# Performance work log

Measured on AMD Instinct MI355X. Metric: run time of the kernel, lower is better.

Reference implementation:

```python
import jax, jax.numpy as jnp
import numpy as np

V, D, M, C, L = 100000, 256, 4096, 4096, 32
PAD = 0
EPS = 1e-8  # torch CosineSimilarity default eps


def setup_inputs() -> dict:
    key = jax.random.key(0)
    ks = jax.random.split(key, 6)
    xs = jax.random.randint(ks[0], (1, L), 0, V)
    mems = jax.random.randint(ks[1], (M, L), 0, V)
    ys = jax.random.randint(ks[2], (1, L), 0, V)
    cands = jax.random.randint(ks[3], (C, L), 0, V)
    lt = jax.random.normal(ks[4], (V, D), dtype=jnp.float32) * 0.02
    lt = lt.at[PAD].set(0.0)  # nn.Embedding padding_idx row is zero
    freqs = jax.random.uniform(ks[5], (V,), dtype=jnp.float32, minval=0.05, maxval=1.0)
    return {"xs": xs, "mems": mems, "ys": ys, "cands": cands, "lt": lt, "freqs": freqs}


def _encode(tokens, lt, freqs):
    # Batched Encoder.forward: freq-weighted average of token embeddings.
    # tokens: [N, L] -> [N, D]
    emb = lt[tokens]                       # [N, L, D] gather
    w = freqs[tokens]                      # [N, L]
    w = w / jnp.linalg.norm(w, axis=1, keepdims=True)  # w * (1 / ||w||)
    return jnp.einsum('nl,nld->nd', w, emb)


def reference(xs, mems, ys, cands, lt, freqs):
    xs_emb = _encode(xs, lt, freqs)                                   # [1, D]
    mems_enc = jnp.concatenate([_encode(mems, lt, freqs), xs_emb], 0)  # [M+1, D]
    # cosine similarity of xs_emb (broadcast) against each memory row
    an = jnp.maximum(jnp.linalg.norm(xs_emb, axis=1), EPS)            # [1]
    bn = jnp.maximum(jnp.linalg.norm(mems_enc, axis=1), EPS)          # [M+1]
    cos = (mems_enc @ xs_emb[0]) / (an * bn)                          # [M+1]
    att = jax.nn.softmax(cos)[None, :]                                # [1, M+1]
    lhs_emb = att @ mems_enc                                          # [1, D]
    ys_emb = _encode(ys, lt, freqs)                                   # [1, D]
    cand_emb = _encode(cands, lt, freqs)                              # [C, D]
    # torch.cat of lhs_emb repeated (1 + C) times; ys then cand encodings
    xs_out = jnp.tile(lhs_emb, (cands.shape[0] + 1, 1))               # [C+1, D]
    ys_out = jnp.concatenate([ys_emb, cand_emb], axis=0)              # [C+1, D]
    return xs_out, ys_out
```

## Files before the change

### kernel.cpp

```cpp
#include <hip/hip_runtime.h>
#include <hip/hip_fp16.h>

#define V_ 100000
#define D_ 256
#define M_ 4096
#define C_ 4096
#define L_ 32
#define ROWS_MEMS (M_ + 1)
#define NTASK (1 + M_ + 1 + C_)

#define LT_ELEMS ((size_t)V_ * D_)
#define HALF_TBL_OFF 4096
#define WS_NEEDED (HALF_TBL_OFF + LT_ELEMS * 2)

__device__ __forceinline__ float wave_allreduce_sum(float v) {
    #pragma unroll
    for (int off = 32; off >= 1; off >>= 1) v += __shfl_xor(v, off, 64);
    return v;
}

__device__ __forceinline__ float lane_bcast_f(float v, int l) {
    return __uint_as_float((unsigned)__builtin_amdgcn_readlane((int)__float_as_uint(v), l));
}

__global__ __launch_bounds__(256) void convert_lt(
    const float4* __restrict__ src, uint2* __restrict__ dst, int n4)
{
    for (int i = blockIdx.x * blockDim.x + threadIdx.x; i < n4;
         i += gridDim.x * blockDim.x) {
        const float4 v = src[i];
        const __half2 h0 = __floats2half2_rn(v.x, v.y);
        const __half2 h1 = __floats2half2_rn(v.z, v.w);
        dst[i] = make_uint2(*(const unsigned*)&h0, *(const unsigned*)&h1);
    }
}

__device__ __forceinline__ float4 encode_row_h(const int* __restrict__ tok_ptr,
                                               const char* __restrict__ lth,
                                               const float* __restrict__ freqs,
                                               const int lane, const unsigned voff) {
    int tok = 0; float w = 0.f;
    if (lane < L_) { tok = tok_ptr[lane]; w = freqs[tok]; }
    const float s2 = wave_allreduce_sum(w * w);
    const float wn = w / sqrtf(s2);

    float4 acc = make_float4(0.f, 0.f, 0.f, 0.f);
    #pragma unroll
    for (int lb = 0; lb < L_; lb += 16) {
        uint2 v[16];
        #pragma unroll
        for (int j = 0; j < 16; ++j) {
            const unsigned t = (unsigned)__builtin_amdgcn_readlane(tok, lb + j);
            v[j] = *reinterpret_cast<const uint2*>(
                lth + t * (unsigned)(D_ * 2) + voff);
        }
        #pragma unroll
        for (int j = 0; j < 16; ++j) {
            const float wl = lane_bcast_f(wn, lb + j);
            const __half2 h0 = *reinterpret_cast<const __half2*>(&v[j].x);
            const __half2 h1 = *reinterpret_cast<const __half2*>(&v[j].y);
            const float2 f0 = __half22float2(h0);
            const float2 f1 = __half22float2(h1);
            acc.x = fmaf(wl, f0.x, acc.x);
            acc.y = fmaf(wl, f0.y, acc.y);
            acc.z = fmaf(wl, f1.x, acc.z);
            acc.w = fmaf(wl, f1.y, acc.w);
        }
    }
    return acc;
}

__device__ __forceinline__ float4 encode_row_f(const int* __restrict__ tok_ptr,
                                               const char* __restrict__ ltb,
                                               const float* __restrict__ freqs,
                                               const int lane, const unsigned voff) {
    int tok = 0; float w = 0.f;
    if (lane < L_) { tok = tok_ptr[lane]; w = freqs[tok]; }
    const float s2 = wave_allreduce_sum(w * w);
    const float wn = w / sqrtf(s2);

    float4 acc = make_float4(0.f, 0.f, 0.f, 0.f);
    #pragma unroll
    for (int lb = 0; lb < L_; lb += 8) {
        float4 v[8];
        #pragma unroll
        for (int j = 0; j < 8; ++j) {
            const unsigned t = (unsigned)__builtin_amdgcn_readlane(tok, lb + j);
            v[j] = *reinterpret_cast<const float4*>(
                ltb + t * (unsigned)(D_ * sizeof(float)) + voff);
        }
        #pragma unroll
        for (int j = 0; j < 8; ++j) {
            const float wl = lane_bcast_f(wn, lb + j);
            acc.x = fmaf(wl, v[j].x, acc.x);
            acc.y = fmaf(wl, v[j].y, acc.y);
            acc.z = fmaf(wl, v[j].z, acc.z);
            acc.w = fmaf(wl, v[j].w, acc.w);
        }
    }
    return acc;
}

template <bool USE_HALF>
__global__ __launch_bounds__(256) void encode_fused(
    const int* __restrict__ xs, const int* __restrict__ mems,
    const int* __restrict__ ys, const int* __restrict__ cands,
    const char* __restrict__ tbl,
    const float* __restrict__ freqs,
    float* __restrict__ lhs_raw,
    float* __restrict__ gsum,
    float* __restrict__ out_ys)
{
    __shared__ float s_xf[D_];
    __shared__ float s_an2;
    __shared__ float s_lred[D_];
    __shared__ float s_ered;

    const int wave = threadIdx.x >> 6;
    const int lane = threadIdx.x & 63;
    const int d0 = lane * 4;
    const unsigned voff = (unsigned)d0 * (USE_HALF ? 2u : 4u);
    const int rt0 = blockIdx.x * 4;
    const bool block_has_att = (rt0 <= M_);

    s_lred[threadIdx.x] = 0.f;
    if (threadIdx.x == 0) s_ered = 0.f;

    if (block_has_att && wave == 0) {
        const float4 xf = USE_HALF ? encode_row_h(xs, tbl, freqs, lane, voff)
                                   : encode_row_f(xs, tbl, freqs, lane, voff);
        *reinterpret_cast<float4*>(&s_xf[d0]) = xf;
        const float an2 = wave_allreduce_sum(xf.x*xf.x + xf.y*xf.y + xf.z*xf.z + xf.w*xf.w);
        if (lane == 0) s_an2 = an2;
    }
    __syncthreads();

    const int rt = rt0 + wave;
    if (rt < NTASK) {
        const int* tok_ptr; float* dst = nullptr; bool has_att = false;
        if (rt == 0) {
            tok_ptr = xs; has_att = true;
        } else if (rt <= M_) {
            tok_ptr = mems + (size_t)(rt - 1) * L_; has_att = true;
        } else if (rt == M_ + 1) {
            tok_ptr = ys; dst = out_ys;
        } else {
            const int c = rt - (M_ + 2);
            tok_ptr = cands + (size_t)c * L_;
            dst = out_ys + (size_t)(c + 1) * D_;
        }

        const float4 acc = USE_HALF ? encode_row_h(tok_ptr, tbl, freqs, lane, voff)
                                    : encode_row_f(tok_ptr, tbl, freqs, lane, voff);

        if (has_att) {
            const float4 xf = *reinterpret_cast<const float4*>(&s_xf[d0]);
            const float d = wave_allreduce_sum(acc.x*xf.x + acc.y*xf.y + acc.z*xf.z + acc.w*xf.w);
            const float q = wave_allreduce_sum(acc.x*acc.x + acc.y*acc.y + acc.z*acc.z + acc.w*acc.w);
            const float an = fmaxf(sqrtf(s_an2), 1e-8f);
            const float bn = fmaxf(sqrtf(q),  1e-8f);
            const float e = expf(d / (an * bn));
            atomicAdd(&s_lred[d0 + 0], e * acc.x);
            atomicAdd(&s_lred[d0 + 1], e * acc.y);
            atomicAdd(&s_lred[d0 + 2], e * acc.z);
            atomicAdd(&s_lred[d0 + 3], e * acc.w);
            if (lane == 0) atomicAdd(&s_ered, e);
        } else {
            *reinterpret_cast<float4*>(dst + d0) = acc;
        }
    }

    if (block_has_att) {
        __syncthreads();
        atomicAdd(&lhs_raw[threadIdx.x], s_lred[threadIdx.x]);
        if (threadIdx.x == 0) atomicAdd(gsum, s_ered);
    }
}

__global__ __launch_bounds__(256) void finalize_tile(
    const float* __restrict__ lhs_raw, const float* __restrict__ gsum,
    float* __restrict__ out_xs)
{
    const float val = lhs_raw[threadIdx.x] / gsum[0];
    for (int r = blockIdx.x; r < ROWS_MEMS; r += gridDim.x)
        out_xs[(size_t)r * D_ + threadIdx.x] = val;
}

extern "C" void kernel_launch(void* const* d_in, const int* in_sizes, int n_in,
                              void* d_out, int out_size, void* d_ws, size_t ws_size,
                              hipStream_t stream) {
    const int*   xs    = (const int*)d_in[0];
    const int*   mems  = (const int*)d_in[1];
    const int*   ys    = (const int*)d_in[2];
    const int*   cands = (const int*)d_in[3];
    const float* lt    = (const float*)d_in[4];
    const float* freqs = (const float*)d_in[5];

    float* out    = (float*)d_out;
    float* out_xs = out;
    float* out_ys = out + (size_t)ROWS_MEMS * D_;

    float* lhs_raw = (float*)d_ws;
    float* gsum    = lhs_raw + D_;
    char*  lt_h    = (char*)d_ws + HALF_TBL_OFF;

    hipMemsetAsync(lhs_raw, 0, (D_ + 1) * sizeof(float), stream);

    if (ws_size >= WS_NEEDED) {
        convert_lt<<<2048, 256, 0, stream>>>(
            (const float4*)lt, (uint2*)lt_h, (int)(LT_ELEMS / 4));
        encode_fused<true><<<(NTASK + 3) / 4, 256, 0, stream>>>(
            xs, mems, ys, cands, lt_h, freqs, lhs_raw, gsum, out_ys);
    } else {
        encode_fused<false><<<(NTASK + 3) / 4, 256, 0, stream>>>(
            xs, mems, ys, cands, (const char*)lt, freqs, lhs_raw, gsum, out_ys);
    }
    finalize_tile<<<1024, 256, 0, stream>>>(lhs_raw, gsum, out_xs);
}
```

Before: 211.6 us.

## Precompute xs encoding once and use 16-byte half loads over paired rows

Adds a single-wave pre-kernel that encodes the query row in fp32, zeroes the accumulators (replacing the memset), and stores the query vector and its squared norm to workspace. Each attention block then reads these instead of re-encoding xs per block. The fp16 gather is restructured so each half-wave loads a full 512-byte row with 16-byte loads, handling two tokens per step, then combines the halves with a cross-half shuffle. The aim is fewer, wider memory transactions and no redundant per-block xs work. The cost is extra shuffles and more registers per lane.

```diff
diff --git a/kernel.cpp b/kernel.cpp
--- a/kernel.cpp
+++ b/kernel.cpp
@@ -10,7 +10,7 @@
 #define NTASK (1 + M_ + 1 + C_)
 
 #define LT_ELEMS ((size_t)V_ * D_)
-#define HALF_TBL_OFF 4096
+#define HALF_TBL_OFF 8192
 #define WS_NEEDED (HALF_TBL_OFF + LT_ELEMS * 2)
 
 __device__ __forceinline__ float wave_allreduce_sum(float v) {
@@ -21,6 +21,45 @@
 
 __device__ __forceinline__ float lane_bcast_f(float v, int l) {
     return __uint_as_float((unsigned)__builtin_amdgcn_readlane((int)__float_as_uint(v), l));
+}
+
+__global__ __launch_bounds__(64) void xs_pre(
+    const int* __restrict__ xs, const float* __restrict__ lt,
+    const float* __restrict__ freqs, float* __restrict__ lhs_raw,
+    float* __restrict__ gsum, float* __restrict__ g_xs)
+{
+    const int lane = threadIdx.x;
+    *reinterpret_cast<float4*>(lhs_raw + lane * 4) = make_float4(0.f, 0.f, 0.f, 0.f);
+    if (lane == 0) *gsum = 0.f;
+
+    int tok = 0; float w = 0.f;
+    if (lane < L_) { tok = xs[lane]; w = freqs[tok]; }
+    const float s2 = wave_allreduce_sum(w * w);
+    const float wn = w / sqrtf(s2);
+
+    const char* ltb = (const char*)lt;
+    const unsigned voff = (unsigned)lane * 16u;
+    float4 acc = make_float4(0.f, 0.f, 0.f, 0.f);
+    #pragma unroll
+    for (int lb = 0; lb < L_; lb += 8) {
+        float4 v[8];
+        #pragma unroll
+        for (int j = 0; j < 8; ++j) {
+            const unsigned t = (unsigned)__builtin_amdgcn_readlane(tok, lb + j);
+            v[j] = *reinterpret_cast<const float4*>(ltb + t * 1024u + voff);
+        }
+        #pragma unroll
+        for (int j = 0; j < 8; ++j) {
+            const float wl = lane_bcast_f(wn, lb + j);
+            acc.x = fmaf(wl, v[j].x, acc.x);
+            acc.y = fmaf(wl, v[j].y, acc.y);
+            acc.z = fmaf(wl, v[j].z, acc.z);
+            acc.w = fmaf(wl, v[j].w, acc.w);
+        }
+    }
+    *reinterpret_cast<float4*>(g_xs + lane * 4) = acc;
+    const float an2 = wave_allreduce_sum(acc.x*acc.x + acc.y*acc.y + acc.z*acc.z + acc.w*acc.w);
+    if (lane == 0) g_xs[256] = an2;
 }
 
 __global__ __launch_bounds__(256) void convert_lt(
@@ -35,103 +74,30 @@
     }
 }
 
-__device__ __forceinline__ float4 encode_row_h(const int* __restrict__ tok_ptr,
-                                               const char* __restrict__ lth,
-                                               const float* __restrict__ freqs,
-                                               const int lane, const unsigned voff) {
-    int tok = 0; float w = 0.f;
-    if (lane < L_) { tok = tok_ptr[lane]; w = freqs[tok]; }
-    const float s2 = wave_allreduce_sum(w * w);
-    const float wn = w / sqrtf(s2);
-
-    float4 acc = make_float4(0.f, 0.f, 0.f, 0.f);
-    #pragma unroll
-    for (int lb = 0; lb < L_; lb += 16) {
-        uint2 v[16];
-        #pragma unroll
-        for (int j = 0; j < 16; ++j) {
-            const unsigned t = (unsigned)__builtin_amdgcn_readlane(tok, lb + j);
-            v[j] = *reinterpret_cast<const uint2*>(
-                lth + t * (unsigned)(D_ * 2) + voff);
-        }
-        #pragma unroll
-        for (int j = 0; j < 16; ++j) {
-            const float wl = lane_bcast_f(wn, lb + j);
-            const __half2 h0 = *reinterpret_cast<const __half2*>(&v[j].x);
-            const __half2 h1 = *reinterpret_cast<const __half2*>(&v[j].y);
-            const float2 f0 = __half22float2(h0);
-            const float2 f1 = __half22float2(h1);
-            acc.x = fmaf(wl, f0.x, acc.x);
-            acc.y = fmaf(wl, f0.y, acc.y);
-            acc.z = fmaf(wl, f1.x, acc.z);
-            acc.w = fmaf(wl, f1.y, acc.w);
-        }
-    }
-    return acc;
-}
-
-__device__ __forceinline__ float4 encode_row_f(const int* __restrict__ tok_ptr,
-                                               const char* __restrict__ ltb,
-                                               const float* __restrict__ freqs,
-                                               const int lane, const unsigned voff) {
-    int tok = 0; float w = 0.f;
-    if (lane < L_) { tok = tok_ptr[lane]; w = freqs[tok]; }
-    const float s2 = wave_allreduce_sum(w * w);
-    const float wn = w / sqrtf(s2);
-
-    float4 acc = make_float4(0.f, 0.f, 0.f, 0.f);
-    #pragma unroll
-    for (int lb = 0; lb < L_; lb += 8) {
-        float4 v[8];
-        #pragma unroll
-        for (int j = 0; j < 8; ++j) {
-            const unsigned t = (unsigned)__builtin_amdgcn_readlane(tok, lb + j);
-            v[j] = *reinterpret_cast<const float4*>(
-                ltb + t * (unsigned)(D_ * sizeof(float)) + voff);
-        }
-        #pragma unroll
-        for (int j = 0; j < 8; ++j) {
-            const float wl = lane_bcast_f(wn, lb + j);
-            acc.x = fmaf(wl, v[j].x, acc.x);
-            acc.y = fmaf(wl, v[j].y, acc.y);
-            acc.z = fmaf(wl, v[j].z, acc.z);
-            acc.w = fmaf(wl, v[j].w, acc.w);
-        }
-    }
-    return acc;
-}
-
-template <bool USE_HALF>
-__global__ __launch_bounds__(256) void encode_fused(
+__global__ __launch_bounds__(256) void encode_fused_h16(
     const int* __restrict__ xs, const int* __restrict__ mems,
     const int* __restrict__ ys, const int* __restrict__ cands,
-    const char* __restrict__ tbl,
-    const float* __restrict__ freqs,
-    float* __restrict__ lhs_raw,
-    float* __restrict__ gsum,
+    const char* __restrict__ lth, const float* __restrict__ freqs,
+    const float* __restrict__ g_xs,
+    float* __restrict__ lhs_raw, float* __restrict__ gsum,
     float* __restrict__ out_ys)
 {
     __shared__ float s_xf[D_];
-    __shared__ float s_an2;
     __shared__ float s_lred[D_];
     __shared__ float s_ered;
-
-    const int wave = threadIdx.x >> 6;
-    const int lane = threadIdx.x & 63;
-    const int d0 = lane * 4;
-    const unsigned voff = (unsigned)d0 * (USE_HALF ? 2u : 4u);
+    __shared__ float s_an2;
+
+    const int tid  = threadIdx.x;
+    const int wave = tid >> 6;
+    const int lane = tid & 63;
     const int rt0 = blockIdx.x * 4;
     const bool block_has_att = (rt0 <= M_);
 
-    s_lred[threadIdx.x] = 0.f;
-    if (threadIdx.x == 0) s_ered = 0.f;
-
-    if (block_has_att && wave == 0) {
-        const float4 xf = USE_HALF ? encode_row_h(xs, tbl, freqs, lane, voff)
-                                   : encode_row_f(xs, tbl, freqs, lane, voff);
-        *reinterpret_cast<float4*>(&s_xf[d0]) = xf;
-        const float an2 = wave_allreduce_sum(xf.x*xf.x + xf.y*xf.y + xf.z*xf.z + xf.w*xf.w);
-        if (lane == 0) s_an2 = an2;
+    s_lred[tid] = 0.f;
+    if (tid == 0) s_ered = 0.f;
+    if (block_has_att) {
+        s_xf[tid] = g_xs[tid];
+        if (tid == 0) s_an2 = g_xs[256];
     }
     __syncthreads();
 
@@ -150,9 +116,150 @@
             dst = out_ys + (size_t)(c + 1) * D_;
         }
 
-        const float4 acc = USE_HALF ? encode_row_h(tok_ptr, tbl, freqs, lane, voff)
-                                    : encode_row_f(tok_ptr, tbl, freqs, lane, voff);
-
+        int tok = 0; float w = 0.f;
+        if (lane < L_) { tok = tok_ptr[lane]; w = freqs[tok]; }
+        const float s2 = wave_allreduce_sum(w * w);
+        const float wn = w / sqrtf(s2);
+
+        const bool lo = (lane < 32);
+        const unsigned inner = (unsigned)(lane & 31) * 16u;
+
+        float acc[8] = {0.f,0.f,0.f,0.f,0.f,0.f,0.f,0.f};
+        #pragma unroll
+        for (int jb = 0; jb < 16; jb += 8) {
+            uint4 v[8];
+            #pragma unroll
+            for (int j = 0; j < 8; ++j) {
+                const unsigned ta = (unsigned)__builtin_amdgcn_readlane(tok, 2*(jb+j));
+                const unsigned tb = (unsigned)__builtin_amdgcn_readlane(tok, 2*(jb+j)+1);
+                const unsigned row = lo ? ta : tb;
+                v[j] = *reinterpret_cast<const uint4*>(lth + row * 512u + inner);
+            }
+            #pragma unroll
+            for (int j = 0; j < 8; ++j) {
+                const float wa = lane_bcast_f(wn, 2*(jb+j));
+                const float wb = lane_bcast_f(wn, 2*(jb+j)+1);
+                const float wl = lo ? wa : wb;
+                const __half2* h = reinterpret_cast<const __half2*>(&v[j]);
+                #pragma unroll
+                for (int k = 0; k < 4; ++k) {
+                    const float2 f = __half22float2(h[k]);
+                    acc[2*k]   = fmaf(wl, f.x, acc[2*k]);
+                    acc[2*k+1] = fmaf(wl, f.y, acc[2*k+1]);
+                }
+            }
+        }
+        #pragma unroll
+        for (int k = 0; k < 8; ++k) acc[k] += __shfl_xor(acc[k], 32, 64);
+
+        const int bq = 8 * (lane & 31);
+        const int bs = bq + (lo ? 0 : 4);
+        const float o0 = lo ? acc[0] : acc[4];
+        const float o1 = lo ? acc[1] : acc[5];
+        const float o2 = lo ? acc[2] : acc[6];
+        const float o3 = lo ? acc[3] : acc[7];
+
+        if (has_att) {
+            const float4 xf0 = *reinterpret_cast<const float4*>(&s_xf[bq]);
+            const float4 xf1 = *reinterpret_cast<const float4*>(&s_xf[bq + 4]);
+            const float pd = acc[0]*xf0.x + acc[1]*xf0.y + acc[2]*xf0.z + acc[3]*xf0.w
+                           + acc[4]*xf1.x + acc[5]*xf1.y + acc[6]*xf1.z + acc[7]*xf1.w;
+            const float pq = acc[0]*acc[0] + acc[1]*acc[1] + acc[2]*acc[2] + acc[3]*acc[3]
+                           + acc[4]*acc[4] + acc[5]*acc[5] + acc[6]*acc[6] + acc[7]*acc[7];
+            const float d = 0.5f * wave_allreduce_sum(pd);
+            const float q = 0.5f * wave_allreduce_sum(pq);
+            const float an = fmaxf(sqrtf(s_an2), 1e-8f);
+            const float bn = fmaxf(sqrtf(q),  1e-8f);
+            const float e = expf(d / (an * bn));
+            atomicAdd(&s_lred[bs + 0], e * o0);
+            atomicAdd(&s_lred[bs + 1], e * o1);
+            atomicAdd(&s_lred[bs + 2], e * o2);
+            atomicAdd(&s_lred[bs + 3], e * o3);
+            if (lane == 0) atomicAdd(&s_ered, e);
+        } else {
+            *reinterpret_cast<float4*>(dst + bs) = make_float4(o0, o1, o2, o3);
+        }
+    }
+
+    if (block_has_att) {
+        __syncthreads();
+        atomicAdd(&lhs_raw[tid], s_lred[tid]);
+        if (tid == 0) atomicAdd(gsum, s_ered);
+    }
+}
+
+__device__ __forceinline__ float4 encode_row_f(const int* __restrict__ tok_ptr,
+                                               const char* __restrict__ ltb,
+                                               const float* __restrict__ freqs,
+                                               const int lane, const unsigned voff) {
+    int tok = 0; float w = 0.f;
+    if (lane < L_) { tok = tok_ptr[lane]; w = freqs[tok]; }
+    const float s2 = wave_allreduce_sum(w * w);
+    const float wn = w / sqrtf(s2);
+    float4 acc = make_float4(0.f, 0.f, 0.f, 0.f);
+    #pragma unroll
+    for (int lb = 0; lb < L_; lb += 8) {
+        float4 v[8];
+        #pragma unroll
+        for (int j = 0; j < 8; ++j) {
+            const unsigned t = (unsigned)__builtin_amdgcn_readlane(tok, lb + j);
+            v[j] = *reinterpret_cast<const float4*>(ltb + t * 1024u + voff);
+        }
+        #pragma unroll
+        for (int j = 0; j < 8; ++j) {
+            const float wl = lane_bcast_f(wn, lb + j);
+            acc.x = fmaf(wl, v[j].x, acc.x);
+            acc.y = fmaf(wl, v[j].y, acc.y);
+            acc.z = fmaf(wl, v[j].z, acc.z);
+            acc.w = fmaf(wl, v[j].w, acc.w);
+        }
+    }
+    return acc;
+}
+
+__global__ __launch_bounds__(256) void encode_fused_f32(
+    const int* __restrict__ xs, const int* __restrict__ mems,
+    const int* __restrict__ ys, const int* __restrict__ cands,
+    const float* __restrict__ lt, const float* __restrict__ freqs,
+    float* __restrict__ lhs_raw, float* __restrict__ gsum,
+    float* __restrict__ out_ys)
+{
+    __shared__ float s_xf[D_];
+    __shared__ float s_an2;
+    __shared__ float s_lred[D_];
+    __shared__ float s_ered;
+
+    const int wave = threadIdx.x >> 6;
+    const int lane = threadIdx.x & 63;
+    const int d0 = lane * 4;
+    const unsigned voff = (unsigned)d0 * 4u;
+    const char* ltb = (const char*)lt;
+    const int rt0 = blockIdx.x * 4;
+    const bool block_has_att = (rt0 <= M_);
+
+    s_lred[threadIdx.x] = 0.f;
+    if (threadIdx.x == 0) s_ered = 0.f;
+
+    if (block_has_att && wave == 0) {
+        const float4 xf = encode_row_f(xs, ltb, freqs, lane, voff);
+        *reinterpret_cast<float4*>(&s_xf[d0]) = xf;
+        const float an2 = wave_allreduce_sum(xf.x*xf.x + xf.y*xf.y + xf.z*xf.z + xf.w*xf.w);
+        if (lane == 0) s_an2 = an2;
+    }
+    __syncthreads();
+
+    const int rt = rt0 + wave;
+    if (rt < NTASK) {
+        const int* tok_ptr; float* dst = nullptr; bool has_att = false;
+        if (rt == 0) { tok_ptr = xs; has_att = true; }
+        else if (rt <= M_) { tok_ptr = mems + (size_t)(rt - 1) * L_; has_att = true; }
+        else if (rt == M_ + 1) { tok_ptr = ys; dst = out_ys; }
+        else {
+            const int c = rt - (M_ + 2);
+            tok_ptr = cands + (size_t)c * L_;
+            dst = out_ys + (size_t)(c + 1) * D_;
+        }
+        const float4 acc = encode_row_f(tok_ptr, ltb, freqs, lane, voff);
         if (has_att) {
             const float4 xf = *reinterpret_cast<const float4*>(&s_xf[d0]);
             const float d = wave_allreduce_sum(acc.x*xf.x + acc.y*xf.y + acc.z*xf.z + acc.w*xf.w);
@@ -202,18 +309,19 @@
 
     float* lhs_raw = (float*)d_ws;
     float* gsum    = lhs_raw + D_;
+    float* g_xs    = gsum + 1;
     char*  lt_h    = (char*)d_ws + HALF_TBL_OFF;
 
-    hipMemsetAsync(lhs_raw, 0, (D_ + 1) * sizeof(float), stream);
-
     if (ws_size >= WS_NEEDED) {
+        xs_pre<<<1, 64, 0, stream>>>(xs, lt, freqs, lhs_raw, gsum, g_xs);
         convert_lt<<<2048, 256, 0, stream>>>(
             (const float4*)lt, (uint2*)lt_h, (int)(LT_ELEMS / 4));
-        encode_fused<true><<<(NTASK + 3) / 4, 256, 0, stream>>>(
-            xs, mems, ys, cands, lt_h, freqs, lhs_raw, gsum, out_ys);
+        encode_fused_h16<<<(NTASK + 3) / 4, 256, 0, stream>>>(
+            xs, mems, ys, cands, lt_h, freqs, g_xs, lhs_raw, gsum, out_ys);
     } else {
-        encode_fused<false><<<(NTASK + 3) / 4, 256, 0, stream>>>(
-            xs, mems, ys, cands, (const char*)lt, freqs, lhs_raw, gsum, out_ys);
+        hipMemsetAsync(lhs_raw, 0, (D_ + 1) * sizeof(float), stream);
+        encode_fused_f32<<<(NTASK + 3) / 4, 256, 0, stream>>>(
+            xs, mems, ys, cands, lt, freqs, lhs_raw, gsum, out_ys);
     }
     finalize_tile<<<1024, 256, 0, stream>>>(lhs_raw, gsum, out_xs);
 }
```

Result: slower. 216.1 us (+2.1%).
